# Optimization experiments

Hardware: AMD Instinct MI355X
Metric: run time of the kernel (lower is better)

## Reference

```python
import jax, jax.numpy as jnp
import numpy as np

DIM = 128      # encoder output dim
D_OUT = 10     # num classes
T = 1.0        # temperature
EPS = 1e-7


def setup_inputs() -> dict:
    key = jax.random.key(0)
    ks = jax.random.split(key, 5)
    B, N, D_IN = 512, 100000, 128
    x = jax.random.normal(ks[0], (B, D_IN), jnp.float32)
    candidate_x = jax.random.normal(ks[1], (N, D_IN), jnp.float32)
    candidate_y = jax.random.randint(ks[2], (N,), 0, D_OUT, dtype=jnp.int32)
    W = jax.random.normal(ks[3], (DIM, D_IN), jnp.float32) / np.sqrt(D_IN).astype(np.float32)
    b = jax.random.normal(ks[4], (DIM,), jnp.float32) * 0.01
    return {"x": x, "candidate_x": candidate_x, "candidate_y": candidate_y, "W": W, "b": b}


def reference(x, candidate_x, candidate_y, W, b):
    # Linear encoder (n_blocks == 0 path)
    h = x @ W.T + b              # [B, DIM]
    hc = candidate_x @ W.T + b   # [N, DIM]
    # Pairwise L2 distances via the Gram expansion (same math as torch.cdist p=2)
    d2 = (jnp.sum(h * h, axis=-1, keepdims=True)
          + jnp.sum(hc * hc, axis=-1)[None, :]
          - 2.0 * (h @ hc.T))    # [B, N]
    dist = jnp.sqrt(jnp.maximum(d2, 0.0)) / T
    # Attention-like masked softmax over candidates (eval: no diagonal mask)
    p = jax.nn.softmax(-dist, axis=-1)              # [B, N]
    onehot_y = jax.nn.one_hot(candidate_y, D_OUT, dtype=p.dtype)  # [N, D_OUT]
    logits = p @ onehot_y                           # [B, D_OUT]
    return jnp.log(logits + EPS)
```

## Files before the change

### kernel.cpp

```cpp
#include <hip/hip_runtime.h>
#include <stdint.h>

typedef __bf16 bf16x8 __attribute__((ext_vector_type(8)));
typedef float f32x4 __attribute__((ext_vector_type(4)));
typedef short short8 __attribute__((ext_vector_type(8)));
typedef unsigned int uint2v __attribute__((ext_vector_type(2)));
typedef float float4_t __attribute__((ext_vector_type(4)));

union FragU { short8 s; bf16x8 b; };
union YbU { uint2v u2[2]; bf16x8 b; };

#define DEVI static __device__ __forceinline__

DEVI f32x4 mfma16(bf16x8 a, bf16x8 b, f32x4 c) {
  return __builtin_amdgcn_mfma_f32_16x16x32_bf16(a, b, c, 0, 0, 0);
}

DEVI bf16x8 cvt8(float4_t a, float4_t b) {
  bf16x8 r;
  r[0] = (__bf16)a[0]; r[1] = (__bf16)a[1]; r[2] = (__bf16)a[2]; r[3] = (__bf16)a[3];
  r[4] = (__bf16)b[0]; r[5] = (__bf16)b[1]; r[6] = (__bf16)b[2]; r[7] = (__bf16)b[3];
  return r;
}

__global__ __launch_bounds__(256) void prep_encode_kernel(
    const float* __restrict__ cx, const float* __restrict__ x,
    const float* __restrict__ W, const float* __restrict__ bias,
    const int* __restrict__ y,
    unsigned short* __restrict__ HC, float* __restrict__ hcn,
    unsigned short* __restrict__ Hm, float* __restrict__ hnm,
    unsigned short* __restrict__ YT,
    int N, int Bm, int NP, int NBA, int NBB, int bpc) {
  __shared__ __align__(16) unsigned short Wl[128 * 128];

  const int bid = blockIdx.x, t = threadIdx.x;
  const int NB_ENC = NBA + NBB;

  if (bid >= NB_ENC) {
    if (bid == NB_ENC) {
      int i = N + t;
      if (i < NP) hcn[i] = 1e30f;
    } else {
      int k = bid - NB_ENC - 1;
      int c = k / bpc, j = k - c * bpc;
      int n0 = j * 2048 + t * 8;
      unsigned short* dst = YT + (size_t)c * NP + n0;
#pragma unroll
      for (int e = 0; e < 8; ++e) {
        int n = n0 + e;
        if (n < NP) dst[e] = (n < N && y[n] == c) ? 0x3F80u : 0u;
      }
    }
    return;
  }

  const float* in;
  unsigned short* outh;
  float* outnorm;
  int M, blk;
  if (bid < NBA) {
    in = cx; outh = HC; outnorm = hcn; M = N; blk = bid;
  } else {
    in = x; outh = Hm; outnorm = hnm; M = Bm; blk = bid - NBA;
  }

  const int lane = t & 63, w = t >> 6;
  const int g = lane >> 4, q = lane & 15;
  const int rowbase = blk * 64 + w * 16;

  float4_t iv[8];
  const int arow = rowbase + q;
  const bool av = arow < M;
  {
    int ar = av ? arow : 0;
#pragma unroll
    for (int kc = 0; kc < 4; ++kc) {
      const float4_t* p = (const float4_t*)(in + (size_t)ar * 128 + kc * 32 + g * 8);
      iv[2 * kc] = p[0];
      iv[2 * kc + 1] = p[1];
    }
  }

  {
    int row = t >> 1, half = t & 1;
    const float* wsrc = W + row * 128 + half * 64;
#pragma unroll
    for (int j = 0; j < 8; ++j) {
      float4_t v0 = *(const float4_t*)(wsrc + j * 8);
      float4_t v1 = *(const float4_t*)(wsrc + j * 8 + 4);
      FragU u; u.b = cvt8(v0, v1);
      int slot = (half * 8 + j) ^ (row & 7);
      *(short8*)((char*)Wl + row * 256 + slot * 16) = u.s;
    }
  }
  __syncthreads();

  bf16x8 a[4];
#pragma unroll
  for (int kc = 0; kc < 4; ++kc) {
    FragU u; u.b = cvt8(iv[2 * kc], iv[2 * kc + 1]);
    if (!av) u.s = short8{0, 0, 0, 0, 0, 0, 0, 0};
    a[kc] = u.b;
  }

  f32x4 acc[8];
#pragma unroll
  for (int nt = 0; nt < 8; ++nt) acc[nt] = f32x4{0.f, 0.f, 0.f, 0.f};
#pragma unroll
  for (int nt = 0; nt < 8; ++nt) {
    int brow = nt * 16 + q;
#pragma unroll
    for (int kc = 0; kc < 4; ++kc) {
      int slot = (kc * 4 + g) ^ (brow & 7);
      FragU u;
      u.s = *(const short8*)((const char*)Wl + brow * 256 + slot * 16);
      acc[nt] = mfma16(a[kc], u.b, acc[nt]);
    }
  }

  float nsq[4] = {0.f, 0.f, 0.f, 0.f};
#pragma unroll
  for (int nt = 0; nt < 8; ++nt) {
    int col = nt * 16 + q;
    float bv = bias[col];
#pragma unroll
    for (int r = 0; r < 4; ++r) {
      int row = rowbase + g * 4 + r;
      float val = acc[nt][r] + bv;
      __bf16 h = (__bf16)val;
      float vf = (float)h;
      nsq[r] += vf * vf;
      union { __bf16 h; unsigned short u; } cv; cv.h = h;
      if (row < M) outh[(size_t)row * 128 + col] = cv.u;
    }
  }
#pragma unroll
  for (int m = 1; m < 16; m <<= 1) {
#pragma unroll
    for (int r = 0; r < 4; ++r) nsq[r] += __shfl_xor(nsq[r], m, 64);
  }
  if (q == 0) {
#pragma unroll
    for (int r = 0; r < 4; ++r) {
      int row = rowbase + g * 4 + r;
      if (row < M) outnorm[row] = nsq[r];
    }
  }
}

__global__ __launch_bounds__(512, 6) void nca_main(
    const unsigned short* __restrict__ H, const float* __restrict__ hnorm,
    const unsigned short* __restrict__ HC, const float* __restrict__ hcnorm,
    const unsigned short* __restrict__ YT, float* __restrict__ part,
    int B, int N, int NP, int NT, int CHUNKS) {
  __shared__ __align__(16) unsigned short HCl[2][64 * 128];

  const int t = threadIdx.x, lane = t & 63, w = t >> 6;
  const int g = lane >> 4, q = lane & 15;
  const int rg = blockIdx.y, chunk = blockIdx.x;
  const int t0 = (int)(((long long)chunk * NT) / CHUNKS);
  const int t1 = (int)(((long long)(chunk + 1) * NT) / CHUNKS);

  bf16x8 hfrag[2][4];
  float hn[2];
  int hrow[2];
#pragma unroll
  for (int s = 0; s < 2; ++s) {
    hrow[s] = rg * 256 + s * 128 + w * 16 + q;
    bool v = hrow[s] < B;
    int ar = v ? hrow[s] : 0;
#pragma unroll
    for (int kc = 0; kc < 4; ++kc) {
      FragU u;
      u.s = *(const short8*)(H + (size_t)ar * 128 + kc * 32 + g * 8);
      if (!v) u.s = short8{0, 0, 0, 0, 0, 0, 0, 0};
      hfrag[s][kc] = u.b;
    }
    hn[s] = hnorm[ar];
  }

  f32x4 pool0 = f32x4{0.f, 0.f, 0.f, 0.f};
  f32x4 pool1 = f32x4{0.f, 0.f, 0.f, 0.f};

#define STAGE(TT, BUF)                                                        \
  {                                                                           \
    _Pragma("unroll") for (int i = 0; i < 2; ++i) {                           \
      int SI = t + 512 * i;                                                   \
      int row = SI >> 4, s = SI & 15;                                         \
      int srcslot = s ^ (row & 7);                                            \
      int cg = (TT)*64 + row;                                                 \
      if (cg >= N) cg = N - 1;                                                \
      const unsigned short* src = HC + (size_t)cg * 128 + srcslot * 8;        \
      char* ldsbase = (char*)HCl[BUF] + w * 1024 + i * 8192;                  \
      __builtin_amdgcn_global_load_lds(                                       \
          (const __attribute__((address_space(1))) unsigned int*)src,         \
          (__attribute__((address_space(3))) unsigned int*)ldsbase, 16, 0, 0);\
    }                                                                         \
  }

  int cur = 0;
  if (t0 < t1) STAGE(t0, 0);

  for (int tt = t0; tt < t1; ++tt) {
    __syncthreads();
    if (tt + 1 < t1) STAGE(tt + 1, cur ^ 1);

    const int colbase = tt * 64;
    float4_t cnv[4];
    uint2v ytu[4];
#pragma unroll
    for (int ns = 0; ns < 4; ++ns) {
      cnv[ns] = *(const float4_t*)(hcnorm + colbase + ns * 16 + g * 4);
      ytu[ns] = *(const uint2v*)(YT + (size_t)q * NP + colbase + ns * 16 + g * 4);
    }

#pragma unroll
    for (int ns = 0; ns < 4; ++ns) {
      int brow = ns * 16 + q;
      f32x4 a0 = f32x4{0.f, 0.f, 0.f, 0.f};
      f32x4 a1 = f32x4{0.f, 0.f, 0.f, 0.f};
#pragma unroll
      for (int kc = 0; kc < 4; ++kc) {
        int slot = (kc * 4 + g) ^ (brow & 7);
        FragU u;
        u.s = *(const short8*)((const char*)HCl[cur] + brow * 256 + slot * 16);
        a0 = mfma16(u.b, hfrag[0][kc], a0);
        a1 = mfma16(u.b, hfrag[1][kc], a1);
      }
      FragU wb0, wb1;
      wb0.s = short8{0, 0, 0, 0, 0, 0, 0, 0};
      wb1.s = short8{0, 0, 0, 0, 0, 0, 0, 0};
#pragma unroll
      for (int r = 0; r < 4; ++r) {
        float d20 = fmaf(-2.f, a0[r], hn[0] + cnv[ns][r]);
        float d21 = fmaf(-2.f, a1[r], hn[1] + cnv[ns][r]);
        d20 = fmaxf(d20, 0.f);
        d21 = fmaxf(d21, 0.f);
        float di0 = __builtin_amdgcn_sqrtf(d20);
        float di1 = __builtin_amdgcn_sqrtf(d21);
        wb0.b[r] = (__bf16)__expf(0.f - di0);
        wb1.b[r] = (__bf16)__expf(0.f - di1);
      }
      YbU yb;
      yb.u2[0] = ytu[ns];
      yb.u2[1] = uint2v{0u, 0u};
      pool0 = mfma16(yb.b, wb0.b, pool0);
      pool1 = mfma16(yb.b, wb1.b, pool1);
    }
    cur ^= 1;
  }
#undef STAGE

  if (hrow[0] < B)
    *(f32x4*)(part + ((size_t)hrow[0] * CHUNKS + chunk) * 16 + g * 4) = pool0;
  if (hrow[1] < B)
    *(f32x4*)(part + ((size_t)hrow[1] * CHUNKS + chunk) * 16 + g * 4) = pool1;
}

__global__ __launch_bounds__(256) void finalize_kernel(
    const float* __restrict__ part, float* __restrict__ out, int B,
    int CHUNKS) {
  const int w = threadIdx.x >> 6, t = threadIdx.x & 63;
  const int row = blockIdx.x * 4 + w;
  if (row >= B) return;
  const int c = t & 15, grp = t >> 4;
  const float* p = part + (size_t)row * CHUNKS * 16;
  float s = 0.f;
  for (int j = grp; j < CHUNKS; j += 4) s += p[j * 16 + c];
  s += __shfl_xor(s, 16, 64);
  s += __shfl_xor(s, 32, 64);
  float Z = 0.f;
#pragma unroll
  for (int cc = 0; cc < 10; ++cc) Z += __shfl(s, cc, 64);
  if (t < 10) out[row * 10 + t] = logf(fmaf(s, 1.f / Z, 1e-7f));
}

extern "C" void kernel_launch(void* const* d_in, const int* in_sizes, int n_in,
                              void* d_out, int out_size, void* d_ws,
                              size_t ws_size, hipStream_t stream) {
  const float* x = (const float*)d_in[0];
  const float* cx = (const float*)d_in[1];
  const int* cy = (const int*)d_in[2];
  const float* W = (const float*)d_in[3];
  const float* b = (const float*)d_in[4];
  const int B = in_sizes[0] / 128;
  const int N = in_sizes[1] / 128;
  float* out = (float*)d_out;

  const int NT = (N + 63) / 64;
  const int NP = NT * 64;
  const int RG = (B + 255) / 256;

  char* ws = (char*)d_ws;
  size_t o = 0;
  auto alloc = [&](size_t bytes) {
    size_t r = o;
    o += (bytes + 255) & ~(size_t)255;
    return r;
  };
  unsigned short* HC = (unsigned short*)(ws + alloc((size_t)N * 128 * 2));
  float* hcn = (float*)(ws + alloc((size_t)NP * 4));
  unsigned short* H = (unsigned short*)(ws + alloc((size_t)B * 128 * 2));
  float* hn = (float*)(ws + alloc((size_t)B * 4));
  unsigned short* YT = (unsigned short*)(ws + alloc((size_t)16 * NP * 2));

  size_t avail = (ws_size > o) ? (ws_size - o) : 0;
  int CHUNKS = (int)(avail / ((size_t)B * 16 * 4));
  if (CHUNKS > 384) CHUNKS = 384;
  if (CHUNKS < 32) CHUNKS = 32;
  float* part = (float*)(ws + alloc((size_t)CHUNKS * B * 16 * 4));

  const int NBA = (N + 63) / 64, NBB = (B + 63) / 64;
  const int bpc = (NP + 2047) / 2048;
  prep_encode_kernel<<<NBA + NBB + 1 + 16 * bpc, 256, 0, stream>>>(
      cx, x, W, b, cy, HC, hcn, H, hn, YT, N, B, NP, NBA, NBB, bpc);

  dim3 grid(CHUNKS, RG);
  nca_main<<<grid, 512, 0, stream>>>(H, hn, HC, hcn, YT, part, B, N, NP, NT,
                                     CHUNKS);
  finalize_kernel<<<(B + 3) / 4, 256, 0, stream>>>(part, out, B, CHUNKS);
}
```

Measured before the change: 184.7 us.

## Fold log2e into encoder, use exp2, batch MFMAs, simplify staging addresses

Scales the encoded features by log2(e) so that distances come out in base-2 units, which lets the main loop call the hardware exp2 directly instead of expf. The main kernel now issues all 16 distance MFMAs before the softmax math, uses precomputed LDS offsets, and drops the per-row clamp in the global-to-LDS staging. The hcn buffer is padded so out-of-range tile reads stay in bounds. Launch bounds and the chunk cap are retuned. Batching the MFMAs raises register pressure, and without the clamp the last tile reads padding past the end of HC.

```diff
diff --git a/kernel.cpp b/kernel.cpp
--- a/kernel.cpp
+++ b/kernel.cpp
@@ -7,6 +7,8 @@
 typedef unsigned int uint2v __attribute__((ext_vector_type(2)));
 typedef float float4_t __attribute__((ext_vector_type(4)));
 
+#define LOG2E 1.44269504088896340736f
+
 union FragU { short8 s; bf16x8 b; };
 union YbU { uint2v u2[2]; bf16x8 b; };
 
@@ -23,7 +25,7 @@
   return r;
 }
 
-__global__ __launch_bounds__(256) void prep_encode_kernel(
+__global__ __launch_bounds__(256, 3) void prep_encode_kernel(
     const float* __restrict__ cx, const float* __restrict__ x,
     const float* __restrict__ W, const float* __restrict__ bias,
     const int* __restrict__ y,
@@ -73,22 +75,23 @@
   const bool av = arow < M;
   {
     int ar = av ? arow : 0;
+    const float* src = in + (size_t)ar * 128 + g * 8;
 #pragma unroll
     for (int kc = 0; kc < 4; ++kc) {
-      const float4_t* p = (const float4_t*)(in + (size_t)ar * 128 + kc * 32 + g * 8);
-      iv[2 * kc] = p[0];
-      iv[2 * kc + 1] = p[1];
+      iv[2 * kc] = *(const float4_t*)(src + kc * 32);
+      iv[2 * kc + 1] = *(const float4_t*)(src + kc * 32 + 4);
     }
   }
 
   {
     int row = t >> 1, half = t & 1;
     const float* wsrc = W + row * 128 + half * 64;
+    float4_t wv[16];
+#pragma unroll
+    for (int j = 0; j < 16; ++j) wv[j] = *(const float4_t*)(wsrc + j * 4);
 #pragma unroll
     for (int j = 0; j < 8; ++j) {
-      float4_t v0 = *(const float4_t*)(wsrc + j * 8);
-      float4_t v1 = *(const float4_t*)(wsrc + j * 8 + 4);
-      FragU u; u.b = cvt8(v0, v1);
+      FragU u; u.b = cvt8(wv[2 * j], wv[2 * j + 1]);
       int slot = (half * 8 + j) ^ (row & 7);
       *(short8*)((char*)Wl + row * 256 + slot * 16) = u.s;
     }
@@ -126,7 +129,7 @@
 #pragma unroll
     for (int r = 0; r < 4; ++r) {
       int row = rowbase + g * 4 + r;
-      float val = acc[nt][r] + bv;
+      float val = (acc[nt][r] + bv) * LOG2E;
       __bf16 h = (__bf16)val;
       float vf = (float)h;
       nsq[r] += vf * vf;
@@ -148,7 +151,7 @@
   }
 }
 
-__global__ __launch_bounds__(512, 6) void nca_main(
+__global__ __launch_bounds__(512, 4) void nca_main(
     const unsigned short* __restrict__ H, const float* __restrict__ hnorm,
     const unsigned short* __restrict__ HC, const float* __restrict__ hcnorm,
     const unsigned short* __restrict__ YT, float* __restrict__ part,
@@ -179,23 +182,31 @@
     hn[s] = hnorm[ar];
   }
 
+  int soff[4];
+#pragma unroll
+  for (int kc = 0; kc < 4; ++kc)
+    soff[kc] = q * 256 + (((kc * 4 + g) ^ (q & 7)) << 4);
+
+  const int srow = t >> 4;
+  const int sslot = (t & 15) ^ (srow & 7);
+  const int g_off = srow * 256 + sslot * 16;
+  const int l_off = w * 1024;
+  const char* HCc = (const char*)HC;
+
   f32x4 pool0 = f32x4{0.f, 0.f, 0.f, 0.f};
   f32x4 pool1 = f32x4{0.f, 0.f, 0.f, 0.f};
 
-#define STAGE(TT, BUF)                                                        \
-  {                                                                           \
-    _Pragma("unroll") for (int i = 0; i < 2; ++i) {                           \
-      int SI = t + 512 * i;                                                   \
-      int row = SI >> 4, s = SI & 15;                                         \
-      int srcslot = s ^ (row & 7);                                            \
-      int cg = (TT)*64 + row;                                                 \
-      if (cg >= N) cg = N - 1;                                                \
-      const unsigned short* src = HC + (size_t)cg * 128 + srcslot * 8;        \
-      char* ldsbase = (char*)HCl[BUF] + w * 1024 + i * 8192;                  \
-      __builtin_amdgcn_global_load_lds(                                       \
-          (const __attribute__((address_space(1))) unsigned int*)src,         \
-          (__attribute__((address_space(3))) unsigned int*)ldsbase, 16, 0, 0);\
-    }                                                                         \
+#define STAGE(TT, BUF)                                                         \
+  {                                                                            \
+    const char* src = HCc + (size_t)(TT)*16384 + g_off;                        \
+    char* lb = (char*)HCl[BUF] + l_off;                                        \
+    __builtin_amdgcn_global_load_lds(                                          \
+        (const __attribute__((address_space(1))) unsigned int*)src,            \
+        (__attribute__((address_space(3))) unsigned int*)lb, 16, 0, 0);        \
+    __builtin_amdgcn_global_load_lds(                                          \
+        (const __attribute__((address_space(1))) unsigned int*)(src + 8192),   \
+        (__attribute__((address_space(3))) unsigned int*)(lb + 8192), 16, 0,   \
+        0);                                                                    \
   }
 
   int cur = 0;
@@ -214,32 +225,39 @@
       ytu[ns] = *(const uint2v*)(YT + (size_t)q * NP + colbase + ns * 16 + g * 4);
     }
 
+    const char* lb = (const char*)HCl[cur];
+    f32x4 a0[4], a1[4];
 #pragma unroll
     for (int ns = 0; ns < 4; ++ns) {
-      int brow = ns * 16 + q;
-      f32x4 a0 = f32x4{0.f, 0.f, 0.f, 0.f};
-      f32x4 a1 = f32x4{0.f, 0.f, 0.f, 0.f};
+      a0[ns] = f32x4{0.f, 0.f, 0.f, 0.f};
+      a1[ns] = f32x4{0.f, 0.f, 0.f, 0.f};
+    }
+#pragma unroll
+    for (int ns = 0; ns < 4; ++ns) {
 #pragma unroll
       for (int kc = 0; kc < 4; ++kc) {
-        int slot = (kc * 4 + g) ^ (brow & 7);
         FragU u;
-        u.s = *(const short8*)((const char*)HCl[cur] + brow * 256 + slot * 16);
-        a0 = mfma16(u.b, hfrag[0][kc], a0);
-        a1 = mfma16(u.b, hfrag[1][kc], a1);
+        u.s = *(const short8*)(lb + soff[kc] + ns * 4096);
+        a0[ns] = mfma16(u.b, hfrag[0][kc], a0[ns]);
+        a1[ns] = mfma16(u.b, hfrag[1][kc], a1[ns]);
       }
+    }
+
+#pragma unroll
+    for (int ns = 0; ns < 4; ++ns) {
       FragU wb0, wb1;
       wb0.s = short8{0, 0, 0, 0, 0, 0, 0, 0};
       wb1.s = short8{0, 0, 0, 0, 0, 0, 0, 0};
 #pragma unroll
       for (int r = 0; r < 4; ++r) {
-        float d20 = fmaf(-2.f, a0[r], hn[0] + cnv[ns][r]);
-        float d21 = fmaf(-2.f, a1[r], hn[1] + cnv[ns][r]);
-        d20 = fmaxf(d20, 0.f);
-        d21 = fmaxf(d21, 0.f);
+        float c0 = hn[0] + cnv[ns][r];
+        float c1 = hn[1] + cnv[ns][r];
+        float d20 = fmaxf(fmaf(-2.f, a0[ns][r], c0), 0.f);
+        float d21 = fmaxf(fmaf(-2.f, a1[ns][r], c1), 0.f);
         float di0 = __builtin_amdgcn_sqrtf(d20);
         float di1 = __builtin_amdgcn_sqrtf(d21);
-        wb0.b[r] = (__bf16)__expf(0.f - di0);
-        wb1.b[r] = (__bf16)__expf(0.f - di1);
+        wb0.b[r] = (__bf16)__builtin_amdgcn_exp2f(-di0);
+        wb1.b[r] = (__bf16)__builtin_amdgcn_exp2f(-di1);
       }
       YbU yb;
       yb.u2[0] = ytu[ns];
@@ -299,14 +317,14 @@
     return r;
   };
   unsigned short* HC = (unsigned short*)(ws + alloc((size_t)N * 128 * 2));
-  float* hcn = (float*)(ws + alloc((size_t)NP * 4));
+  float* hcn = (float*)(ws + alloc((size_t)NP * 4 + 16384));
   unsigned short* H = (unsigned short*)(ws + alloc((size_t)B * 128 * 2));
   float* hn = (float*)(ws + alloc((size_t)B * 4));
   unsigned short* YT = (unsigned short*)(ws + alloc((size_t)16 * NP * 2));
 
   size_t avail = (ws_size > o) ? (ws_size - o) : 0;
   int CHUNKS = (int)(avail / ((size_t)B * 16 * 4));
-  if (CHUNKS > 384) CHUNKS = 384;
+  if (CHUNKS > 256) CHUNKS = 256;
   if (CHUNKS < 32) CHUNKS = 32;
   float* part = (float*)(ws + alloc((size_t)CHUNKS * B * 16 * 4));
 
```

New measurement: 162.3 us. -12.1%, faster.
